# Performance work log

Hardware: AMD Instinct MI355X
Metric: run time of the kernel (lower is better)

## Reference

```python
import jax, jax.numpy as jnp
import numpy as np

D_MODEL = 2048
D_FF = 4 * D_MODEL  # 8192, GPT-2 MLP convention
TOTAL = D_MODEL * D_FF          # elements per weight matrix
L = TOTAL // 2                  # complex FFT length (real/imag interleaved pairs)
NUM_COEFFS = 16
BATCH, SEQ = 2, 4096


def _decompress(coeffs_real, coeffs_imag, indices, shape, scale):
    """Faithful port of FastPoincareFourier.decompress_matrix.
    Scatter K complex coeffs into a length-L zero buffer, ifft, then
    de-interleave real/imag back into a flat real vector of length 2L == TOTAL.
    """
    coeffs = jax.lax.complex(coeffs_real, coeffs_imag)
    full_fft = jnp.zeros((L,), dtype=jnp.complex64).at[indices].set(coeffs)
    restored = jnp.fft.ifft(full_fft)  # [L] complex
    # stack([real, imag], dim=1).flatten() -> interleaved [2L]
    flat = jnp.stack([jnp.real(restored), jnp.imag(restored)], axis=1).reshape(-1)
    # 2L == TOTAL exactly (TOTAL is even), so no trunc/pad needed
    return flat.reshape(shape) * scale  # scale broadcasts ([1])


def setup_inputs() -> dict:
    key = jax.random.key(0)
    ks = jax.random.split(key, 12)
    # coefficients scaled by L*0.02 so ifft (which divides by L) yields ~N(0,0.02) weights
    cscale = L * 0.02
    return {
        "x": jax.random.normal(ks[0], (BATCH, SEQ, D_MODEL), dtype=jnp.float32),
        "fc_coeffs_real": jax.random.normal(ks[1], (NUM_COEFFS,), dtype=jnp.float32) * cscale,
        "fc_coeffs_imag": jax.random.normal(ks[2], (NUM_COEFFS,), dtype=jnp.float32) * cscale,
        "fc_scale": jax.random.uniform(ks[3], (1,), dtype=jnp.float32) + 0.5,
        "proj_coeffs_real": jax.random.normal(ks[4], (NUM_COEFFS,), dtype=jnp.float32) * cscale,
        "proj_coeffs_imag": jax.random.normal(ks[5], (NUM_COEFFS,), dtype=jnp.float32) * cscale,
        "proj_scale": jax.random.uniform(ks[6], (1,), dtype=jnp.float32) + 0.5,
        "c_fc_bias": jax.random.normal(ks[7], (D_FF,), dtype=jnp.float32) * 0.02,
        "c_proj_bias": jax.random.normal(ks[8], (D_MODEL,), dtype=jnp.float32) * 0.02,
        "fc_indices": jax.random.randint(ks[9], (NUM_COEFFS,), 0, L, dtype=jnp.int64),
        "proj_indices": jax.random.randint(ks[10], (NUM_COEFFS,), 0, L, dtype=jnp.int64),
    }


def reference(x, fc_coeffs_real, fc_coeffs_imag, fc_scale,
              proj_coeffs_real, proj_coeffs_imag, proj_scale,
              c_fc_bias, c_proj_bias, fc_indices, proj_indices):
    # W_fc: [d_model, d_ff]; F.linear(x, W.T) == x @ W
    w_fc = _decompress(fc_coeffs_real, fc_coeffs_imag, fc_indices, (D_MODEL, D_FF), fc_scale)
    h = jnp.einsum('bsd,df->bsf', x, w_fc) + c_fc_bias
    h = jax.nn.gelu(h, approximate=False)  # nn.GELU() default = exact erf
    # W_proj: [d_ff, d_model]
    w_proj = _decompress(proj_coeffs_real, proj_coeffs_imag, proj_indices, (D_FF, D_MODEL), proj_scale)
    out = jnp.einsum('bsf,fd->bsd', h, w_proj) + c_proj_bias
    return out
```

## Files before the change

kernel.cpp:

```cpp
#include <hip/hip_runtime.h>
#include <stdint.h>


typedef short bfrag8 __attribute__((ext_vector_type(8)));
typedef short bfrag4 __attribute__((ext_vector_type(4)));
typedef float f32x4  __attribute__((ext_vector_type(4)));

#define LMASK 8388607u
#define TWO_PI_OVER_L 7.4901405658478575e-7f

__device__ __forceinline__ unsigned short f2bf(float f) {
    unsigned u = __float_as_uint(f);
    u = (u + 0x7FFFu + ((u >> 16) & 1u)) >> 16;
    return (unsigned short)u;
}
__device__ __forceinline__ float bf2f(unsigned short h) {
    unsigned u = ((unsigned)h) << 16;
    return __builtin_bit_cast(float, u);
}
__device__ __forceinline__ unsigned pk2bf(float a, float b) {
    unsigned ua = __float_as_uint(a) + 0x8000u;
    unsigned ub = __float_as_uint(b) + 0x8000u;
    return __builtin_amdgcn_perm(ub, ua, 0x07060302u);
}
__device__ __forceinline__ float gelu_fast(float x) {
    float xx = x * x;
    float p  = fmaf(xx, 0.044715f, 1.0f);
    float t  = (x * p) * -2.3022083f;
    float e  = __builtin_amdgcn_exp2f(t);
    return x * __builtin_amdgcn_rcpf(1.0f + e);
}

#if defined(__has_builtin)
#if __has_builtin(__builtin_amdgcn_mfma_f32_16x16x16bf16_1k)
#define HAVE_MFMA16_1K 1
#endif
#endif
__device__ __forceinline__ void mfma16(f32x4& acc, bfrag4 a, bfrag4 b) {
#ifdef HAVE_MFMA16_1K
    acc = __builtin_amdgcn_mfma_f32_16x16x16bf16_1k(a, b, acc, 0, 0, 0);
#else
    asm("v_mfma_f32_16x16x16_bf16 %0, %1, %2, %0" : "+v"(acc) : "v"(a), "v"(b));
#endif
}

__device__ __forceinline__ void vt_body(const int* __restrict__ idx,
                                        unsigned short* __restrict__ out, int j) {
    unsigned m = ((unsigned)j) >> 1;
    int p = j & 1;
    #pragma unroll
    for (int k = 0; k < 16; ++k) {
        unsigned s  = ((unsigned)idx[k]) & LMASK;
        unsigned ph = (s * m) & LMASK;
        float sn, cs;
        __sincosf((float)ph * TWO_PI_OVER_L, &sn, &cs);
        float e0 = p ? sn : cs;
        float e1 = p ? cs : -sn;
        out[(size_t)j * 32 + 2 * k]     = f2bf(e0);
        out[(size_t)j * 32 + 2 * k + 1] = f2bf(e1);
    }
}

__global__ void k_build(const float* __restrict__ fcr, const float* __restrict__ fci,
                        const int* __restrict__ fidx, const float* __restrict__ fcs,
                        const float* __restrict__ prr, const float* __restrict__ pri,
                        const int* __restrict__ pidx, const float* __restrict__ prs,
                        unsigned short* __restrict__ ufct, unsigned short* __restrict__ vtfc,
                        unsigned short* __restrict__ u2t,  unsigned short* __restrict__ vprt) {
    int b = blockIdx.x, t = threadIdx.x;
    if (b < 8) {
        int i = b * 256 + t;
        float sc = fcs[0] * (1.0f / 8388608.0f);
        #pragma unroll
        for (int k = 0; k < 16; ++k) {
            int v = fidx[k];
            bool keep = true;
            for (int j = k + 1; j < 16; ++j) keep = keep && (fidx[j] != v);
            unsigned s  = (((unsigned)v) << 12) & LMASK;
            unsigned ph = (s * (unsigned)i) & LMASK;
            float sn, cs;
            __sincosf((float)ph * TWO_PI_OVER_L, &sn, &cs);
            float a = keep ? fcr[k] * sc : 0.0f;
            float bb = keep ? fci[k] * sc : 0.0f;
            ufct[(size_t)(2 * k) * 2048 + i]     = f2bf(a * cs - bb * sn);
            ufct[(size_t)(2 * k + 1) * 2048 + i] = f2bf(a * sn + bb * cs);
        }
    } else if (b < 40) {
        vt_body(fidx, vtfc, (b - 8) * 256 + t);
    } else if (b < 72) {
        int f = (b - 40) * 256 + t;
        float sc = prs[0] * (1.0f / 8388608.0f);
        #pragma unroll
        for (int k = 0; k < 16; ++k) {
            int v = pidx[k];
            bool keep = true;
            for (int j = k + 1; j < 16; ++j) keep = keep && (pidx[j] != v);
            unsigned s  = (((unsigned)v) << 10) & LMASK;
            unsigned ph = (s * (unsigned)f) & LMASK;
            float sn, cs;
            __sincosf((float)ph * TWO_PI_OVER_L, &sn, &cs);
            float a = keep ? prr[k] * sc : 0.0f;
            float bb = keep ? pri[k] * sc : 0.0f;
            u2t[(size_t)(2 * k) * 8192 + f]     = f2bf(a * cs - bb * sn);
            u2t[(size_t)(2 * k + 1) * 8192 + f] = f2bf(a * sn + bb * cs);
        }
    } else {
        vt_body(pidx, vprt, (b - 72) * 256 + t);
    }
}

__global__ __launch_bounds__(512, 4) void k_t1(
    const float* __restrict__ x,
    const unsigned short* __restrict__ ufct,
    unsigned short* __restrict__ t1)
{
    __shared__ float red[8 * 512];
    const int tid  = threadIdx.x;
    const int w    = tid >> 6;
    const int lane = tid & 63;
    const int lr   = lane & 15;
    const int hi   = lane >> 4;
    const size_t tok0 = (size_t)blockIdx.x * 16;

    f32x4 acc[2];
    { f32x4 z = {0.f,0.f,0.f,0.f}; acc[0] = z; acc[1] = z; }
    #pragma unroll 4
    for (int s = 0; s < 8; ++s) {
        int k = w * 256 + s * 32 + hi * 8;
        const float* xp = x + (tok0 + lr) * 2048 + k;
        float4 v0 = *(const float4*)xp;
        float4 v1 = *(const float4*)(xp + 4);
        uint4 aw = make_uint4(pk2bf(v0.x, v0.y), pk2bf(v0.z, v0.w),
                              pk2bf(v1.x, v1.y), pk2bf(v1.z, v1.w));
        bfrag8 af = __builtin_bit_cast(bfrag8, aw);
        bfrag8 b0 = *(const bfrag8*)(ufct + (size_t)lr * 2048 + k);
        bfrag8 b1 = *(const bfrag8*)(ufct + (size_t)(16 + lr) * 2048 + k);
        acc[0] = __builtin_amdgcn_mfma_f32_16x16x32_bf16(af, b0, acc[0], 0, 0, 0);
        acc[1] = __builtin_amdgcn_mfma_f32_16x16x32_bf16(af, b1, acc[1], 0, 0, 0);
    }
    #pragma unroll
    for (int nj = 0; nj < 2; ++nj)
        #pragma unroll
        for (int r = 0; r < 4; ++r)
            red[w * 512 + (hi * 4 + r) * 32 + nj * 16 + lr] = acc[nj][r];
    __syncthreads();
    float s = 0.f;
    #pragma unroll
    for (int w2 = 0; w2 < 8; ++w2) s += red[w2 * 512 + tid];
    t1[(size_t)blockIdx.x * 512 + tid] = f2bf(s);
}

__global__ __launch_bounds__(512, 4) void k_mid(
    const unsigned short* __restrict__ t1,
    const unsigned short* __restrict__ vtfc,
    const unsigned short* __restrict__ u2t,
    const float* __restrict__ fcb,
    unsigned short* __restrict__ t2p)
{
    __shared__ float red[2 * 8 * 512];
    const int tid  = threadIdx.x;
    const int w    = tid >> 6;
    const int lane = tid & 63;
    const int lr   = lane & 15;
    const int hi   = lane >> 4;
    const int fc   = blockIdx.x;
    const int g0   = blockIdx.y * 16;

    bfrag8 va0[2], va1[2];
    bfrag4 u00[2], u01[2], u10[2], u11[2];
    f32x4  cb0[2], cb1[2];
    #pragma unroll
    for (int sl = 0; sl < 2; ++sl) {
        int fb = fc * 512 + w * 64 + sl * 32;
        va0[sl] = *(const bfrag8*)(vtfc + (size_t)(fb + lr) * 32 + hi * 8);
        va1[sl] = *(const bfrag8*)(vtfc + (size_t)(fb + 16 + lr) * 32 + hi * 8);
        cb0[sl] = *(const f32x4*)(fcb + fb + hi * 4);
        cb1[sl] = *(const f32x4*)(fcb + fb + 16 + hi * 4);
        u00[sl] = *(const bfrag4*)(u2t + (size_t)lr * 8192 + fb + 4 * hi);
        u01[sl] = *(const bfrag4*)(u2t + (size_t)lr * 8192 + fb + 16 + 4 * hi);
        u10[sl] = *(const bfrag4*)(u2t + (size_t)(16 + lr) * 8192 + fb + 4 * hi);
        u11[sl] = *(const bfrag4*)(u2t + (size_t)(16 + lr) * 8192 + fb + 16 + 4 * hi);
    }
    const int toff = lr * 32 + hi * 8;

    #pragma unroll 1
    for (int pi = 0; pi < 8; ++pi) {
        int ga = g0 + pi * 2, gb = ga + 1;
        bfrag8 tA = *(const bfrag8*)(t1 + (size_t)ga * 512 + toff);
        bfrag8 tB = *(const bfrag8*)(t1 + (size_t)gb * 512 + toff);
        f32x4 aA0 = {0.f,0.f,0.f,0.f}, aA1 = {0.f,0.f,0.f,0.f};
        f32x4 aB0 = {0.f,0.f,0.f,0.f}, aB1 = {0.f,0.f,0.f,0.f};
        #pragma unroll
        for (int sl = 0; sl < 2; ++sl) {
            f32x4 sA0 = __builtin_amdgcn_mfma_f32_16x16x32_bf16(va0[sl], tA, cb0[sl], 0, 0, 0);
            f32x4 sB0 = __builtin_amdgcn_mfma_f32_16x16x32_bf16(va0[sl], tB, cb0[sl], 0, 0, 0);
            f32x4 sA1 = __builtin_amdgcn_mfma_f32_16x16x32_bf16(va1[sl], tA, cb1[sl], 0, 0, 0);
            f32x4 sB1 = __builtin_amdgcn_mfma_f32_16x16x32_bf16(va1[sl], tB, cb1[sl], 0, 0, 0);
            uint2 hA0 = make_uint2(pk2bf(gelu_fast(sA0[0]), gelu_fast(sA0[1])),
                                   pk2bf(gelu_fast(sA0[2]), gelu_fast(sA0[3])));
            uint2 hB0 = make_uint2(pk2bf(gelu_fast(sB0[0]), gelu_fast(sB0[1])),
                                   pk2bf(gelu_fast(sB0[2]), gelu_fast(sB0[3])));
            uint2 hA1 = make_uint2(pk2bf(gelu_fast(sA1[0]), gelu_fast(sA1[1])),
                                   pk2bf(gelu_fast(sA1[2]), gelu_fast(sA1[3])));
            uint2 hB1 = make_uint2(pk2bf(gelu_fast(sB1[0]), gelu_fast(sB1[1])),
                                   pk2bf(gelu_fast(sB1[2]), gelu_fast(sB1[3])));
            bfrag4 fA0 = __builtin_bit_cast(bfrag4, hA0);
            bfrag4 fB0 = __builtin_bit_cast(bfrag4, hB0);
            bfrag4 fA1 = __builtin_bit_cast(bfrag4, hA1);
            bfrag4 fB1 = __builtin_bit_cast(bfrag4, hB1);
            mfma16(aA0, u00[sl], fA0);
            mfma16(aB0, u00[sl], fB0);
            mfma16(aA1, u10[sl], fA0);
            mfma16(aB1, u10[sl], fB0);
            mfma16(aA0, u01[sl], fA1);
            mfma16(aB0, u01[sl], fB1);
            mfma16(aA1, u11[sl], fA1);
            mfma16(aB1, u11[sl], fB1);
        }
        #pragma unroll
        for (int r = 0; r < 4; ++r) {
            int r2a = hi * 4 + r, r2b = 16 + hi * 4 + r;
            red[(0 * 8 + w) * 512 + lr * 32 + ((r2a + lr) & 31)] = aA0[r];
            red[(0 * 8 + w) * 512 + lr * 32 + ((r2b + lr) & 31)] = aA1[r];
            red[(1 * 8 + w) * 512 + lr * 32 + ((r2a + lr) & 31)] = aB0[r];
            red[(1 * 8 + w) * 512 + lr * 32 + ((r2b + lr) & 31)] = aB1[r];
        }
        __syncthreads();
        {
            int tok = tid >> 5, rr = tid & 31;
            int slot = tok * 32 + ((rr + tok) & 31);
            float sa = 0.f, sb = 0.f;
            #pragma unroll
            for (int w2 = 0; w2 < 8; ++w2) {
                sa += red[(0 * 8 + w2) * 512 + slot];
                sb += red[(1 * 8 + w2) * 512 + slot];
            }
            t2p[((size_t)fc * 512 + ga) * 512 + tid] = f2bf(sa);
            t2p[((size_t)fc * 512 + gb) * 512 + tid] = f2bf(sb);
        }
        __syncthreads();
    }
}

__global__ __launch_bounds__(512, 4) void k_out(
    const unsigned short* __restrict__ t2p,
    const unsigned short* __restrict__ vprt,
    const float* __restrict__ prb,
    float* __restrict__ out)
{
    __shared__ unsigned short lT[512];
    const int tid  = threadIdx.x;
    const int w    = tid >> 6;
    const int lane = tid & 63;
    const int lr   = lane & 15;
    const int hi   = lane >> 4;
    const int g    = blockIdx.x;
    const size_t tok0 = (size_t)g * 16;

    {
        float s = 0.f;
        #pragma unroll
        for (int c = 0; c < 16; ++c)
            s += bf2f(t2p[((size_t)c * 512 + g) * 512 + tid]);
        lT[tid] = f2bf(s);
    }
    __syncthreads();
    const bfrag8 t2a = *(const bfrag8*)(lT + lr * 32 + hi * 8);
    #pragma unroll 4
    for (int nj = 0; nj < 16; ++nj) {
        int d = w * 256 + nj * 16 + lr;
        bfrag8 vp = *(const bfrag8*)(vprt + (size_t)d * 32 + hi * 8);
        float bn = prb[d];
        f32x4 c = {bn, bn, bn, bn};
        f32x4 o = __builtin_amdgcn_mfma_f32_16x16x32_bf16(t2a, vp, c, 0, 0, 0);
        #pragma unroll
        for (int r = 0; r < 4; ++r)
            out[(tok0 + hi * 4 + r) * 2048 + d] = o[r];
    }
}

extern "C" void kernel_launch(void* const* d_in, const int* in_sizes, int n_in,
                              void* d_out, int out_size, void* d_ws, size_t ws_size,
                              hipStream_t stream) {
    (void)in_sizes; (void)n_in; (void)out_size; (void)ws_size;
    const float* x   = (const float*)d_in[0];
    const float* fcr = (const float*)d_in[1];
    const float* fci = (const float*)d_in[2];
    const float* fcs = (const float*)d_in[3];
    const float* prr = (const float*)d_in[4];
    const float* pri = (const float*)d_in[5];
    const float* prs = (const float*)d_in[6];
    const float* fcb = (const float*)d_in[7];
    const float* prb = (const float*)d_in[8];
    const int* fidx  = (const int*)d_in[9];
    const int* pidx  = (const int*)d_in[10];
    float* out = (float*)d_out;
    char* ws = (char*)d_ws;

    size_t off = 0;
    auto take = [&](size_t bytes) { size_t p = off; off = (off + bytes + 255) & ~(size_t)255; return p; };
    unsigned short* ufct = (unsigned short*)(ws + take((size_t)32 * 2048 * 2));
    unsigned short* vtfc = (unsigned short*)(ws + take((size_t)8192 * 32 * 2));
    unsigned short* u2t  = (unsigned short*)(ws + take((size_t)32 * 8192 * 2));
    unsigned short* vprt = (unsigned short*)(ws + take((size_t)2048 * 32 * 2));
    unsigned short* t1   = (unsigned short*)(ws + take((size_t)8192 * 32 * 2));
    unsigned short* t2p  = (unsigned short*)(ws + take((size_t)16 * 8192 * 32 * 2));

    k_build<<<dim3(80), 256, 0, stream>>>(fcr, fci, fidx, fcs, prr, pri, pidx, prs,
                                          ufct, vtfc, u2t, vprt);
    k_t1 <<<dim3(512),    512, 0, stream>>>(x, ufct, t1);
    k_mid<<<dim3(16, 32), 512, 0, stream>>>(t1, vtfc, u2t, fcb, t2p);
    k_out<<<dim3(512),    512, 0, stream>>>(t2p, vprt, prb, out);
}
```

Before: 74.52 us.

## Fuse low-rank factor generation into consumer kernels, drop k_build launch

Removes the separate k_build kernel and computes the DFT-derived bf16 factor fragments (U_fc, V_fc, U_proj, V_proj) on the fly inside k_t1, k_mid and k_out using sincos. This eliminates one kernel launch, its serialization point and the global round-trip of the factor tables. In exchange every block recomputes the trig values redundantly, which adds a large amount of transcendental ALU work per block, especially in k_t1 where 16 sincos calls are done per MFMA pair.

```diff
diff --git a/kernel.cpp b/kernel.cpp
--- a/kernel.cpp
+++ b/kernel.cpp
@@ -29,6 +29,9 @@
     float t  = (x * p) * -2.3022083f;
     float e  = __builtin_amdgcn_exp2f(t);
     return x * __builtin_amdgcn_rcpf(1.0f + e);
+}
+__device__ __forceinline__ void sc_ph(unsigned ph, float& sn, float& cs) {
+    __sincosf((float)ph * TWO_PI_OVER_L, &sn, &cs);
 }
 
 #if defined(__has_builtin)
@@ -44,74 +47,17 @@
 #endif
 }
 
-__device__ __forceinline__ void vt_body(const int* __restrict__ idx,
-                                        unsigned short* __restrict__ out, int j) {
-    unsigned m = ((unsigned)j) >> 1;
-    int p = j & 1;
-    #pragma unroll
-    for (int k = 0; k < 16; ++k) {
-        unsigned s  = ((unsigned)idx[k]) & LMASK;
-        unsigned ph = (s * m) & LMASK;
-        float sn, cs;
-        __sincosf((float)ph * TWO_PI_OVER_L, &sn, &cs);
-        float e0 = p ? sn : cs;
-        float e1 = p ? cs : -sn;
-        out[(size_t)j * 32 + 2 * k]     = f2bf(e0);
-        out[(size_t)j * 32 + 2 * k + 1] = f2bf(e1);
-    }
-}
-
-__global__ void k_build(const float* __restrict__ fcr, const float* __restrict__ fci,
-                        const int* __restrict__ fidx, const float* __restrict__ fcs,
-                        const float* __restrict__ prr, const float* __restrict__ pri,
-                        const int* __restrict__ pidx, const float* __restrict__ prs,
-                        unsigned short* __restrict__ ufct, unsigned short* __restrict__ vtfc,
-                        unsigned short* __restrict__ u2t,  unsigned short* __restrict__ vprt) {
-    int b = blockIdx.x, t = threadIdx.x;
-    if (b < 8) {
-        int i = b * 256 + t;
-        float sc = fcs[0] * (1.0f / 8388608.0f);
-        #pragma unroll
-        for (int k = 0; k < 16; ++k) {
-            int v = fidx[k];
-            bool keep = true;
-            for (int j = k + 1; j < 16; ++j) keep = keep && (fidx[j] != v);
-            unsigned s  = (((unsigned)v) << 12) & LMASK;
-            unsigned ph = (s * (unsigned)i) & LMASK;
-            float sn, cs;
-            __sincosf((float)ph * TWO_PI_OVER_L, &sn, &cs);
-            float a = keep ? fcr[k] * sc : 0.0f;
-            float bb = keep ? fci[k] * sc : 0.0f;
-            ufct[(size_t)(2 * k) * 2048 + i]     = f2bf(a * cs - bb * sn);
-            ufct[(size_t)(2 * k + 1) * 2048 + i] = f2bf(a * sn + bb * cs);
-        }
-    } else if (b < 40) {
-        vt_body(fidx, vtfc, (b - 8) * 256 + t);
-    } else if (b < 72) {
-        int f = (b - 40) * 256 + t;
-        float sc = prs[0] * (1.0f / 8388608.0f);
-        #pragma unroll
-        for (int k = 0; k < 16; ++k) {
-            int v = pidx[k];
-            bool keep = true;
-            for (int j = k + 1; j < 16; ++j) keep = keep && (pidx[j] != v);
-            unsigned s  = (((unsigned)v) << 10) & LMASK;
-            unsigned ph = (s * (unsigned)f) & LMASK;
-            float sn, cs;
-            __sincosf((float)ph * TWO_PI_OVER_L, &sn, &cs);
-            float a = keep ? prr[k] * sc : 0.0f;
-            float bb = keep ? pri[k] * sc : 0.0f;
-            u2t[(size_t)(2 * k) * 8192 + f]     = f2bf(a * cs - bb * sn);
-            u2t[(size_t)(2 * k + 1) * 8192 + f] = f2bf(a * sn + bb * cs);
-        }
-    } else {
-        vt_body(pidx, vprt, (b - 72) * 256 + t);
-    }
+__device__ __forceinline__ bool keep_coef(const int* __restrict__ idx, int kk) {
+    int v = idx[kk];
+    bool keep = true;
+    for (int j = kk + 1; j < 16; ++j) keep = keep && (idx[j] != v);
+    return keep;
 }
 
 __global__ __launch_bounds__(512, 4) void k_t1(
     const float* __restrict__ x,
-    const unsigned short* __restrict__ ufct,
+    const float* __restrict__ fcr, const float* __restrict__ fci,
+    const int* __restrict__ fidx,  const float* __restrict__ fcs,
     unsigned short* __restrict__ t1)
 {
     __shared__ float red[8 * 512];
@@ -122,9 +68,21 @@
     const int hi   = lane >> 4;
     const size_t tok0 = (size_t)blockIdx.x * 16;
 
+    const float sc = fcs[0] * (1.0f / 8388608.0f);
+    const int p   = lr & 1;
+    const int kk0 = lr >> 1, kk1 = 8 + (lr >> 1);
+    unsigned s0, s1; float a0, b0, a1, b1;
+    {
+        bool k0 = keep_coef(fidx, kk0), k1 = keep_coef(fidx, kk1);
+        s0 = (((unsigned)fidx[kk0]) << 12) & LMASK;
+        s1 = (((unsigned)fidx[kk1]) << 12) & LMASK;
+        a0 = k0 ? fcr[kk0] * sc : 0.f;  b0 = k0 ? fci[kk0] * sc : 0.f;
+        a1 = k1 ? fcr[kk1] * sc : 0.f;  b1 = k1 ? fci[kk1] * sc : 0.f;
+    }
+
     f32x4 acc[2];
     { f32x4 z = {0.f,0.f,0.f,0.f}; acc[0] = z; acc[1] = z; }
-    #pragma unroll 4
+    #pragma unroll 2
     for (int s = 0; s < 8; ++s) {
         int k = w * 256 + s * 32 + hi * 8;
         const float* xp = x + (tok0 + lr) * 2048 + k;
@@ -133,10 +91,23 @@
         uint4 aw = make_uint4(pk2bf(v0.x, v0.y), pk2bf(v0.z, v0.w),
                               pk2bf(v1.x, v1.y), pk2bf(v1.z, v1.w));
         bfrag8 af = __builtin_bit_cast(bfrag8, aw);
-        bfrag8 b0 = *(const bfrag8*)(ufct + (size_t)lr * 2048 + k);
-        bfrag8 b1 = *(const bfrag8*)(ufct + (size_t)(16 + lr) * 2048 + k);
-        acc[0] = __builtin_amdgcn_mfma_f32_16x16x32_bf16(af, b0, acc[0], 0, 0, 0);
-        acc[1] = __builtin_amdgcn_mfma_f32_16x16x32_bf16(af, b1, acc[1], 0, 0, 0);
+        float e0[8], e1[8];
+        #pragma unroll
+        for (int t = 0; t < 8; ++t) {
+            float sn, cs;
+            sc_ph((s0 * (unsigned)(k + t)) & LMASK, sn, cs);
+            e0[t] = p ? fmaf(a0, sn, b0 * cs) : fmaf(a0, cs, -b0 * sn);
+            sc_ph((s1 * (unsigned)(k + t)) & LMASK, sn, cs);
+            e1[t] = p ? fmaf(a1, sn, b1 * cs) : fmaf(a1, cs, -b1 * sn);
+        }
+        uint4 bw0 = make_uint4(pk2bf(e0[0], e0[1]), pk2bf(e0[2], e0[3]),
+                               pk2bf(e0[4], e0[5]), pk2bf(e0[6], e0[7]));
+        uint4 bw1 = make_uint4(pk2bf(e1[0], e1[1]), pk2bf(e1[2], e1[3]),
+                               pk2bf(e1[4], e1[5]), pk2bf(e1[6], e1[7]));
+        bfrag8 bf0 = __builtin_bit_cast(bfrag8, bw0);
+        bfrag8 bf1 = __builtin_bit_cast(bfrag8, bw1);
+        acc[0] = __builtin_amdgcn_mfma_f32_16x16x32_bf16(af, bf0, acc[0], 0, 0, 0);
+        acc[1] = __builtin_amdgcn_mfma_f32_16x16x32_bf16(af, bf1, acc[1], 0, 0, 0);
     }
     #pragma unroll
     for (int nj = 0; nj < 2; ++nj)
@@ -152,8 +123,10 @@
 
 __global__ __launch_bounds__(512, 4) void k_mid(
     const unsigned short* __restrict__ t1,
-    const unsigned short* __restrict__ vtfc,
-    const unsigned short* __restrict__ u2t,
+    const int* __restrict__ fidx,
+    const int* __restrict__ pidx,
+    const float* __restrict__ prr, const float* __restrict__ pri,
+    const float* __restrict__ prs,
     const float* __restrict__ fcb,
     unsigned short* __restrict__ t2p)
 {
@@ -165,21 +138,70 @@
     const int hi   = lane >> 4;
     const int fc   = blockIdx.x;
     const int g0   = blockIdx.y * 16;
+    const int fb_w = fc * 512 + w * 64;
 
     bfrag8 va0[2], va1[2];
-    bfrag4 u00[2], u01[2], u10[2], u11[2];
     f32x4  cb0[2], cb1[2];
+    unsigned skv[4];
+    #pragma unroll
+    for (int c = 0; c < 4; ++c) skv[c] = ((unsigned)fidx[hi * 4 + c]) & LMASK;
     #pragma unroll
     for (int sl = 0; sl < 2; ++sl) {
-        int fb = fc * 512 + w * 64 + sl * 32;
-        va0[sl] = *(const bfrag8*)(vtfc + (size_t)(fb + lr) * 32 + hi * 8);
-        va1[sl] = *(const bfrag8*)(vtfc + (size_t)(fb + 16 + lr) * 32 + hi * 8);
+        #pragma unroll
+        for (int rv = 0; rv < 2; ++rv) {
+            int j = fb_w + sl * 32 + rv * 16 + lr;
+            unsigned m = ((unsigned)j) >> 1;
+            int pj = j & 1;
+            float v[8];
+            #pragma unroll
+            for (int c = 0; c < 4; ++c) {
+                float sn, cs;
+                sc_ph((skv[c] * m) & LMASK, sn, cs);
+                v[2 * c]     = pj ? sn : cs;
+                v[2 * c + 1] = pj ? cs : -sn;
+            }
+            uint4 pw = make_uint4(pk2bf(v[0], v[1]), pk2bf(v[2], v[3]),
+                                  pk2bf(v[4], v[5]), pk2bf(v[6], v[7]));
+            if (rv == 0) va0[sl] = __builtin_bit_cast(bfrag8, pw);
+            else         va1[sl] = __builtin_bit_cast(bfrag8, pw);
+        }
+        int fb = fb_w + sl * 32;
         cb0[sl] = *(const f32x4*)(fcb + fb + hi * 4);
         cb1[sl] = *(const f32x4*)(fcb + fb + 16 + hi * 4);
-        u00[sl] = *(const bfrag4*)(u2t + (size_t)lr * 8192 + fb + 4 * hi);
-        u01[sl] = *(const bfrag4*)(u2t + (size_t)lr * 8192 + fb + 16 + 4 * hi);
-        u10[sl] = *(const bfrag4*)(u2t + (size_t)(16 + lr) * 8192 + fb + 4 * hi);
-        u11[sl] = *(const bfrag4*)(u2t + (size_t)(16 + lr) * 8192 + fb + 16 + 4 * hi);
+    }
+
+    bfrag4 u00[2], u01[2], u10[2], u11[2];
+    {
+        const float scp = prs[0] * (1.0f / 8388608.0f);
+        const int pp = lr & 1;
+        #pragma unroll
+        for (int rv = 0; rv < 2; ++rv) {
+            int kk = rv * 8 + (lr >> 1);
+            bool kp = keep_coef(pidx, kk);
+            unsigned s = (((unsigned)pidx[kk]) << 10) & LMASK;
+            float a = kp ? prr[kk] * scp : 0.f;
+            float b = kp ? pri[kk] * scp : 0.f;
+            #pragma unroll
+            for (int sl = 0; sl < 2; ++sl) {
+                #pragma unroll
+                for (int hf = 0; hf < 2; ++hf) {
+                    unsigned f0 = (unsigned)(fb_w + sl * 32 + hf * 16 + 4 * hi);
+                    float v[4];
+                    #pragma unroll
+                    for (int t = 0; t < 4; ++t) {
+                        float sn, cs;
+                        sc_ph((s * (f0 + t)) & LMASK, sn, cs);
+                        v[t] = pp ? fmaf(a, sn, b * cs) : fmaf(a, cs, -b * sn);
+                    }
+                    uint2 pw = make_uint2(pk2bf(v[0], v[1]), pk2bf(v[2], v[3]));
+                    bfrag4 fr = __builtin_bit_cast(bfrag4, pw);
+                    if      (rv == 0 && hf == 0) u00[sl] = fr;
+                    else if (rv == 0 && hf == 1) u01[sl] = fr;
+                    else if (rv == 1 && hf == 0) u10[sl] = fr;
+                    else                         u11[sl] = fr;
+                }
+            }
+        }
     }
     const int toff = lr * 32 + hi * 8;
 
@@ -244,7 +266,7 @@
 
 __global__ __launch_bounds__(512, 4) void k_out(
     const unsigned short* __restrict__ t2p,
-    const unsigned short* __restrict__ vprt,
+    const int* __restrict__ pidx,
     const float* __restrict__ prb,
     float* __restrict__ out)
 {
@@ -264,15 +286,30 @@
             s += bf2f(t2p[((size_t)c * 512 + g) * 512 + tid]);
         lT[tid] = f2bf(s);
     }
+    unsigned skv[4];
+    #pragma unroll
+    for (int c = 0; c < 4; ++c) skv[c] = ((unsigned)pidx[hi * 4 + c]) & LMASK;
     __syncthreads();
     const bfrag8 t2a = *(const bfrag8*)(lT + lr * 32 + hi * 8);
     #pragma unroll 4
     for (int nj = 0; nj < 16; ++nj) {
         int d = w * 256 + nj * 16 + lr;
-        bfrag8 vp = *(const bfrag8*)(vprt + (size_t)d * 32 + hi * 8);
+        unsigned m = ((unsigned)d) >> 1;
+        int pd = d & 1;
+        float v[8];
+        #pragma unroll
+        for (int c = 0; c < 4; ++c) {
+            float sn, cs;
+            sc_ph((skv[c] * m) & LMASK, sn, cs);
+            v[2 * c]     = pd ? sn : cs;
+            v[2 * c + 1] = pd ? cs : -sn;
+        }
+        uint4 pw = make_uint4(pk2bf(v[0], v[1]), pk2bf(v[2], v[3]),
+                              pk2bf(v[4], v[5]), pk2bf(v[6], v[7]));
+        bfrag8 vp = __builtin_bit_cast(bfrag8, pw);
         float bn = prb[d];
-        f32x4 c = {bn, bn, bn, bn};
-        f32x4 o = __builtin_amdgcn_mfma_f32_16x16x32_bf16(t2a, vp, c, 0, 0, 0);
+        f32x4 c4 = {bn, bn, bn, bn};
+        f32x4 o = __builtin_amdgcn_mfma_f32_16x16x32_bf16(t2a, vp, c4, 0, 0, 0);
         #pragma unroll
         for (int r = 0; r < 4; ++r)
             out[(tok0 + hi * 4 + r) * 2048 + d] = o[r];
@@ -299,16 +336,10 @@
 
     size_t off = 0;
     auto take = [&](size_t bytes) { size_t p = off; off = (off + bytes + 255) & ~(size_t)255; return p; };
-    unsigned short* ufct = (unsigned short*)(ws + take((size_t)32 * 2048 * 2));
-    unsigned short* vtfc = (unsigned short*)(ws + take((size_t)8192 * 32 * 2));
-    unsigned short* u2t  = (unsigned short*)(ws + take((size_t)32 * 8192 * 2));
-    unsigned short* vprt = (unsigned short*)(ws + take((size_t)2048 * 32 * 2));
-    unsigned short* t1   = (unsigned short*)(ws + take((size_t)8192 * 32 * 2));
-    unsigned short* t2p  = (unsigned short*)(ws + take((size_t)16 * 8192 * 32 * 2));
-
-    k_build<<<dim3(80), 256, 0, stream>>>(fcr, fci, fidx, fcs, prr, pri, pidx, prs,
-                                          ufct, vtfc, u2t, vprt);
-    k_t1 <<<dim3(512),    512, 0, stream>>>(x, ufct, t1);
-    k_mid<<<dim3(16, 32), 512, 0, stream>>>(t1, vtfc, u2t, fcb, t2p);
-    k_out<<<dim3(512),    512, 0, stream>>>(t2p, vprt, prb, out);
-}
+    unsigned short* t1  = (unsigned short*)(ws + take((size_t)8192 * 32 * 2));
+    unsigned short* t2p = (unsigned short*)(ws + take((size_t)16 * 8192 * 32 * 2));
+
+    k_t1 <<<dim3(512),    512, 0, stream>>>(x, fcr, fci, fidx, fcs, t1);
+    k_mid<<<dim3(16, 32), 512, 0, stream>>>(t1, fidx, pidx, prr, pri, prs, fcb, t2p);
+    k_out<<<dim3(512),    512, 0, stream>>>(t2p, pidx, prb, out);
+}
```

After: 76.90 us. 3.2% more time.
